# Performance work log

Hardware: AMD Instinct MI355X
Metric: run time of the kernel (lower is better)

Reference implementation:

```python
import jax, jax.numpy as jnp
import numpy as np

NEG_SLOPE = 0.01  # torch F.leaky_relu default


def setup_inputs() -> dict:
    key = jax.random.key(0)
    k1, k2, k3, k4 = jax.random.split(key, 4)
    N, E, R, D = 100000, 1250000, 16, 64
    ego_embed = jax.random.normal(k1, (N, D), dtype=jnp.float32) * 0.1
    relation_weights = jax.random.normal(k2, (R, D, D), dtype=jnp.float32) * (1.0 / np.sqrt(D))
    edge_index = jax.random.randint(k3, (2, E), 0, N, dtype=jnp.int32)
    edge_type = jax.random.randint(k4, (E,), 0, R, dtype=jnp.int32)
    return {"ego_embed": ego_embed, "relation_weights": relation_weights,
            "edge_index": edge_index, "edge_type": edge_type}


def reference(ego_embed, relation_weights, edge_index, edge_type):
    head, tail = edge_index[0], edge_index[1]
    n_entities = ego_embed.shape[0]
    # Transform every node by every relation once ([R,N,D]) instead of
    # materializing the per-edge [E,D,D] weight gather the torch bmm implies;
    # same math: transformed_head[e] = ego_embed[head[e]] @ W[edge_type[e]].
    transformed_all = jnp.einsum('nd,rdk->rnk', ego_embed, relation_weights)
    transformed_head = transformed_all[edge_type, head]        # [E, D]
    tail_emb = ego_embed[tail]                                  # [E, D]
    scores = jax.nn.leaky_relu(jnp.sum(transformed_head * tail_emb, axis=1),
                               negative_slope=NEG_SLOPE)        # [E]
    exp_scores = jnp.exp(scores)                                # unnormalized attention
    denom = jax.ops.segment_sum(exp_scores, head, num_segments=n_entities)[head]
    norm_att = exp_scores / denom                               # segment softmax
    weighted = tail_emb * norm_att[:, None]                     # [E, D]
    # scatter_mean: segment sum / per-segment edge count (clamped to 1)
    summed = jax.ops.segment_sum(weighted, head, num_segments=n_entities)
    counts = jax.ops.segment_sum(jnp.ones_like(exp_scores), head, num_segments=n_entities)
    return summed / jnp.maximum(counts, 1.0)[:, None]
```

## Files before the change

kernel.cpp:

```cpp
#include <hip/hip_runtime.h>
#include <stdint.h>

#define NEG_SLOPE 0.01f
#define HPG 32
#define TSTR 72
#define BSH 8
#define NBMAX 512
#define K1CH 8192
#define CAP2 8192

typedef float f32x4 __attribute__((ext_vector_type(4)));
typedef short short8 __attribute__((ext_vector_type(8)));
typedef unsigned int u32;

#define DPPADD(v, ctrl) ((v) + __int_as_float(__builtin_amdgcn_update_dpp( \
        0, __float_as_int(v), (ctrl), 0xF, 0xF, true)))

__device__ inline short f2bf(float f) {
    union { float f; uint32_t u; } x; x.f = f;
    uint32_t r = x.u + 0x7FFF + ((x.u >> 16) & 1);
    return (short)(r >> 16);
}
__device__ inline float bf2f(unsigned short u) {
    union { uint32_t u; float f; } x; x.u = ((uint32_t)u) << 16; return x.f;
}

__global__ void __launch_bounds__(512) kA(
        const int* __restrict__ head, const int* __restrict__ tail,
        const int* __restrict__ etype, int E, int NB, int nblk,
        u32* __restrict__ staging, int* bucket_cur,
        const float* __restrict__ ego, unsigned short* __restrict__ ego_bf,
        int NE8, const float* __restrict__ rw, short* __restrict__ wfrag,
        int* __restrict__ head_off, int N) {
    int t = threadIdx.x;
    int bid = blockIdx.x;
    if (bid < nblk) {
        __shared__ int lcnt[NBMAX], lbase[NBMAX], lfill[NBMAX];
        for (int b = t; b < NBMAX; b += 512) lcnt[b] = 0;
        __syncthreads();
        long long base = (long long)bid * K1CH;
        short mybk[K1CH / 512];
        u32 myrec[K1CH / 512];
        #pragma unroll
        for (int s = 0; s < K1CH / 512; ++s) {
            long long e = base + t + s * 512;
            int bk = -1; u32 rec = 0;
            if (e < E) {
                int h = head[e];
                bk = h >> BSH;
                rec = (u32)tail[e] | ((u32)etype[e] << 20) | ((u32)(h & 255) << 24);
                atomicAdd(&lcnt[bk], 1);
            }
            mybk[s] = (short)bk; myrec[s] = rec;
        }
        __syncthreads();
        for (int b = t; b < NB; b += 512) {
            int c = lcnt[b];
            lbase[b] = c ? atomicAdd(&bucket_cur[b], c) : 0;
            lfill[b] = 0;
        }
        __syncthreads();
        #pragma unroll
        for (int s = 0; s < K1CH / 512; ++s) {
            int bk = mybk[s];
            if (bk >= 0) {
                int rk = atomicAdd(&lfill[bk], 1);
                int pos = lbase[bk] + rk;
                if (pos >= CAP2) pos = CAP2 - 1;
                staging[(size_t)bk * CAP2 + pos] = myrec[s];
            }
        }
    } else {
        int ib = bid - nblk;
        if (ib == 0 && t == 0) head_off[N] = E;
        if (ib < 16) {
            int r = ib;
            int lane = t & 63;
            int c = lane & 15, q = lane >> 4;
            int pair = t >> 6;
            int t4 = pair >> 1, kh = pair & 1;
            int m = t4 * 16 + c;
            short8 f;
            for (int j = 0; j < 8; ++j) {
                int k = kh * 32 + q * 8 + j;
                f[j] = f2bf(rw[r * 4096 + k * 64 + m]);
            }
            *(short8*)(wfrag + ((size_t)((r * 4 + t4) * 2 + kh) * 64 + lane) * 8) = f;
        }
        int i = ib * 512 + t;
        if (i < NE8) {
            const float4* p = (const float4*)ego + (size_t)i * 2;
            float4 a = p[0], b = p[1];
            short8 v;
            v[0] = f2bf(a.x); v[1] = f2bf(a.y); v[2] = f2bf(a.z); v[3] = f2bf(a.w);
            v[4] = f2bf(b.x); v[5] = f2bf(b.y); v[6] = f2bf(b.z); v[7] = f2bf(b.w);
            *(short8*)(ego_bf + (size_t)i * 8) = v;
        }
    }
}

__global__ void __launch_bounds__(512) kB(
        const u32* __restrict__ staging, const int* __restrict__ bucket_cur,
        int* __restrict__ head_off, int* __restrict__ recs2, int N, int NB) {
    __shared__ int pre[NBMAX];
    __shared__ int lcnt[256], lofs[256], lfill[256];
    __shared__ u32 lrec[CAP2];
    int t = threadIdx.x;
    int b = blockIdx.x;
    if (t < 256) lcnt[t] = 0;
    int v = (t < NB) ? bucket_cur[t] : 0;
    pre[t] = v;
    __syncthreads();
    for (int off = 1; off < 512; off <<= 1) {
        int x = (t >= off) ? pre[t - off] : 0;
        __syncthreads();
        pre[t] += x;
        __syncthreads();
    }
    int cnt_raw = bucket_cur[b];
    int base_g = pre[b] - cnt_raw;
    int cntb = cnt_raw > CAP2 ? CAP2 : cnt_raw;
    int hbase = b << BSH;
    const u32* sb = staging + (size_t)b * CAP2;
    for (int t0 = t; t0 < cntb; t0 += 512) {
        u32 rec = sb[t0];
        lrec[t0] = rec;
        atomicAdd(&lcnt[rec >> 24], 1);
    }
    __syncthreads();
    if (t < 64) {
        int cl[4]; int cs = 0;
        #pragma unroll
        for (int j = 0; j < 4; ++j) { cl[j] = lcnt[t * 4 + j]; cs += cl[j]; }
        int inc = cs;
        for (int off = 1; off < 64; off <<= 1) {
            int u = __shfl_up(inc, off);
            if (t >= off) inc += u;
        }
        int run = inc - cs;
        #pragma unroll
        for (int j = 0; j < 4; ++j) {
            lofs[t * 4 + j] = run; lfill[t * 4 + j] = run; run += cl[j];
        }
    }
    __syncthreads();
    if (t < 256 && hbase + t < N)
        head_off[hbase + t] = base_g + lofs[t];
    for (int t0 = t; t0 < cntb; t0 += 512) {
        u32 rec = lrec[t0];
        int rk = atomicAdd(&lfill[rec >> 24], 1);
        recs2[base_g + rk] = (int)(rec & 0xFFFFFF);
    }
}

__global__ void __launch_bounds__(512, 4) k4_fused(
        const unsigned short* __restrict__ ego_bf,
        const short* __restrict__ wfrag,
        const int* __restrict__ recs2,
        const int* __restrict__ head_off,
        float* __restrict__ out, int N) {
    __shared__ unsigned short T[16 * HPG * TSTR];
    int tid = threadIdx.x;
    int wave = tid >> 6;
    int lane = tid & 63;
    int c = lane & 15, q = lane >> 4;
    int hb = blockIdx.x * HPG;

    for (int t = 0; t < 2; ++t) {
        int r = wave * 2 + t;
        const short* wp = wfrag + (size_t)r * 4096;
        short8 wf[4][2];
        #pragma unroll
        for (int t4 = 0; t4 < 4; ++t4)
            #pragma unroll
            for (int kh = 0; kh < 2; ++kh)
                wf[t4][kh] = *(const short8*)(wp + ((size_t)((t4 * 2 + kh) * 64 + lane)) * 8);
        #pragma unroll
        for (int hf = 0; hf < 2; ++hf) {
            int hrow = hb + hf * 16 + c;
            if (hrow >= N) hrow = N - 1;
            const unsigned short* hr = ego_bf + (size_t)hrow * 64;
            short8 b0 = *(const short8*)(hr + q * 8);
            short8 b1 = *(const short8*)(hr + 32 + q * 8);
            #pragma unroll
            for (int t4 = 0; t4 < 4; ++t4) {
                f32x4 a = {0.f, 0.f, 0.f, 0.f};
                a = __builtin_amdgcn_mfma_f32_16x16x32_bf16(wf[t4][0], b0, a, 0, 0, 0);
                a = __builtin_amdgcn_mfma_f32_16x16x32_bf16(wf[t4][1], b1, a, 0, 0, 0);
                ushort4 us;
                us.x = (unsigned short)f2bf(a[0]);
                us.y = (unsigned short)f2bf(a[1]);
                us.z = (unsigned short)f2bf(a[2]);
                us.w = (unsigned short)f2bf(a[3]);
                *(ushort4*)&T[(size_t)(r * HPG + hf * 16 + c) * TSTR + t4 * 16 + q * 4] = us;
            }
        }
    }
    __syncthreads();

    int hql = wave * 4 + q;
    int h = hb + hql;
    if (h >= N) return;
    int lq = c;
    int g2 = lq >> 3, c8 = lq & 7;
    int qb = q * 16;
    int s0 = head_off[h], s1 = head_off[h + 1];
    int cnt = s1 - s0;
    int nbt = (cnt + 15) >> 4;
    float acc[8] = {0.f, 0.f, 0.f, 0.f, 0.f, 0.f, 0.f, 0.f};
    float den = 0.f;

    auto loadRec = [&](int b) -> int {
        if (b >= nbt) return 0;
        int idx = s0 + b * 16 + lq;
        return (idx < s1) ? recs2[idx] : 0;
    };

    int rjA[8]; short8 rowsA[8];
    int recL1;
    {
        int recL0 = loadRec(0);
        #pragma unroll
        for (int j = 0; j < 8; ++j) rjA[j] = __shfl(recL0, qb + j * 2 + g2);
        #pragma unroll
        for (int j = 0; j < 8; ++j)
            rowsA[j] = *(const short8*)(ego_bf + (size_t)(rjA[j] & 0xFFFFF) * 64 + c8 * 8);
        recL1 = loadRec(1);
    }
    for (int b = 0; b < nbt; ++b) {
        int recL2 = loadRec(b + 2);
        int rjB[8]; short8 rowsB[8];
        #pragma unroll
        for (int j = 0; j < 8; ++j) rjB[j] = __shfl(recL1, qb + j * 2 + g2);
        #pragma unroll
        for (int j = 0; j < 8; ++j)
            rowsB[j] = *(const short8*)(ego_bf + (size_t)(rjB[j] & 0xFFFFF) * 64 + c8 * 8);
        int ng = s1 - (s0 + b * 16); if (ng > 16) ng = 16;
        #pragma unroll
        for (int sIt = 0; sIt < 8; ++sIt) {
            if (sIt * 2 < ng) {
                short8 trw = *(const short8*)&T[(size_t)(((u32)rjA[sIt] >> 20) * HPG + hql) * TSTR + c8 * 8];
                float rf[8];
                float sa = 0.f, sb = 0.f;
                #pragma unroll
                for (int k = 0; k < 4; ++k) {
                    rf[k] = bf2f((unsigned short)rowsA[sIt][k]);
                    sa += rf[k] * bf2f((unsigned short)trw[k]);
                }
                #pragma unroll
                for (int k = 4; k < 8; ++k) {
                    rf[k] = bf2f((unsigned short)rowsA[sIt][k]);
                    sb += rf[k] * bf2f((unsigned short)trw[k]);
                }
                float s = sa + sb;
                s = DPPADD(s, 0xB1);
                s = DPPADD(s, 0x4E);
                s = DPPADD(s, 0x141);
                float lr = s > 0.f ? s : NEG_SLOPE * s;
                float w = (sIt * 2 + g2 < ng) ? __expf(lr) : 0.f;
                den += w;
                #pragma unroll
                for (int k = 0; k < 8; ++k) acc[k] += w * rf[k];
            }
        }
        recL1 = recL2;
        #pragma unroll
        for (int j = 0; j < 8; ++j) { rjA[j] = rjB[j]; rowsA[j] = rowsB[j]; }
    }
    den = DPPADD(den, 0x128);
    #pragma unroll
    for (int k = 0; k < 8; ++k) acc[k] = DPPADD(acc[k], 0x128);
    if (g2 == 0) {
        float sc = (cnt > 0) ? 1.f / (den * (float)cnt) : 0.f;
        float4 v0 = {acc[0] * sc, acc[1] * sc, acc[2] * sc, acc[3] * sc};
        float4 v1 = {acc[4] * sc, acc[5] * sc, acc[6] * sc, acc[7] * sc};
        float* op = out + (size_t)h * 64 + c8 * 8;
        *(float4*)op = v0;
        *(float4*)(op + 4) = v1;
    }
}

extern "C" void kernel_launch(void* const* d_in, const int* in_sizes, int n_in,
                              void* d_out, int out_size, void* d_ws, size_t ws_size,
                              hipStream_t stream) {
    const float* ego = (const float*)d_in[0];
    const float* rw  = (const float*)d_in[1];
    const int* eidx  = (const int*)d_in[2];
    const int* etyp  = (const int*)d_in[3];
    int N = in_sizes[0] / 64;
    int E = in_sizes[3];
    const int* head = eidx;
    const int* tail = eidx + E;
    float* out = (float*)d_out;

    char* ws = (char*)d_ws;
    size_t o = 0;
    auto take = [&](size_t bytes) -> char* {
        char* p = ws + o;
        o = (o + bytes + 255) & ~(size_t)255;
        return p;
    };
    int NB = (N + (1 << BSH) - 1) >> BSH;
    if (NB > NBMAX) NB = NBMAX;
    int nblk = (E + K1CH - 1) / K1CH;
    int NE8 = N * 8;
    int nbI = (NE8 + 511) / 512;
    if (nbI < 16) nbI = 16;
    unsigned short* ego_bf = (unsigned short*)take((size_t)N * 64 * 2);
    short* wfrag    = (short*)take(16 * 4096 * 2);
    int* recs2      = (int*)take((size_t)E * 4);
    u32* staging    = (u32*)take((size_t)NB * CAP2 * 4);
    int* bucket_cur = (int*)take(NBMAX * 4);
    int* head_off   = (int*)take((size_t)(N + 1) * 4);
    (void)ws_size; (void)n_in; (void)out_size;

    hipMemsetAsync(bucket_cur, 0, NBMAX * 4, stream);
    kA<<<nblk + nbI, 512, 0, stream>>>(head, tail, etyp, E, NB, nblk,
                                       staging, bucket_cur,
                                       ego, ego_bf, NE8, rw, wfrag,
                                       head_off, N);
    kB<<<NB, 512, 0, stream>>>(staging, bucket_cur, head_off, recs2, N, NB);
    k4_fused<<<(N + HPG - 1) / HPG, 512, 0, stream>>>(ego_bf, wfrag, recs2,
                                                      head_off, out, N);
}
```

Measured before the change: 180.0 us.

## Halve heads per block and split each head's edges across two lane groups

Each block now covers 16 heads instead of 32, which halves the shared-memory transform table and raises the occupancy hint from 4 to 8 blocks. Each head's edge list is split between two 16-lane groups, and their partial softmax denominators and accumulators are combined with a cross-lane shuffle. This shortens the per-head serial loop and evens out load across degree-skewed heads. In exchange, the per-block 16x64x64 weight MFMA work and the weight-fragment loads are amortized over half as many heads, and the cross-group reduction adds a little overhead.

```diff
diff --git a/kernel.cpp b/kernel.cpp
--- a/kernel.cpp
+++ b/kernel.cpp
@@ -2,7 +2,7 @@
 #include <stdint.h>
 
 #define NEG_SLOPE 0.01f
-#define HPG 32
+#define HPG 16
 #define TSTR 72
 #define BSH 8
 #define NBMAX 512
@@ -153,7 +153,7 @@
     }
 }
 
-__global__ void __launch_bounds__(512, 4) k4_fused(
+__global__ void __launch_bounds__(512, 8) k4_fused(
         const unsigned short* __restrict__ ego_bf,
         const short* __restrict__ wfrag,
         const int* __restrict__ recs2,
@@ -175,45 +175,46 @@
             #pragma unroll
             for (int kh = 0; kh < 2; ++kh)
                 wf[t4][kh] = *(const short8*)(wp + ((size_t)((t4 * 2 + kh) * 64 + lane)) * 8);
-        #pragma unroll
-        for (int hf = 0; hf < 2; ++hf) {
-            int hrow = hb + hf * 16 + c;
-            if (hrow >= N) hrow = N - 1;
-            const unsigned short* hr = ego_bf + (size_t)hrow * 64;
-            short8 b0 = *(const short8*)(hr + q * 8);
-            short8 b1 = *(const short8*)(hr + 32 + q * 8);
-            #pragma unroll
-            for (int t4 = 0; t4 < 4; ++t4) {
-                f32x4 a = {0.f, 0.f, 0.f, 0.f};
-                a = __builtin_amdgcn_mfma_f32_16x16x32_bf16(wf[t4][0], b0, a, 0, 0, 0);
-                a = __builtin_amdgcn_mfma_f32_16x16x32_bf16(wf[t4][1], b1, a, 0, 0, 0);
-                ushort4 us;
-                us.x = (unsigned short)f2bf(a[0]);
-                us.y = (unsigned short)f2bf(a[1]);
-                us.z = (unsigned short)f2bf(a[2]);
-                us.w = (unsigned short)f2bf(a[3]);
-                *(ushort4*)&T[(size_t)(r * HPG + hf * 16 + c) * TSTR + t4 * 16 + q * 4] = us;
-            }
+        int hrow = hb + c;
+        if (hrow >= N) hrow = N - 1;
+        const unsigned short* hr = ego_bf + (size_t)hrow * 64;
+        short8 b0 = *(const short8*)(hr + q * 8);
+        short8 b1 = *(const short8*)(hr + 32 + q * 8);
+        #pragma unroll
+        for (int t4 = 0; t4 < 4; ++t4) {
+            f32x4 a = {0.f, 0.f, 0.f, 0.f};
+            a = __builtin_amdgcn_mfma_f32_16x16x32_bf16(wf[t4][0], b0, a, 0, 0, 0);
+            a = __builtin_amdgcn_mfma_f32_16x16x32_bf16(wf[t4][1], b1, a, 0, 0, 0);
+            ushort4 us;
+            us.x = (unsigned short)f2bf(a[0]);
+            us.y = (unsigned short)f2bf(a[1]);
+            us.z = (unsigned short)f2bf(a[2]);
+            us.w = (unsigned short)f2bf(a[3]);
+            *(ushort4*)&T[(size_t)(r * HPG + c) * TSTR + t4 * 16 + q * 4] = us;
         }
     }
     __syncthreads();
 
-    int hql = wave * 4 + q;
+    int hql = wave * 2 + (q >> 1);
+    int halfsel = q & 1;
     int h = hb + hql;
-    if (h >= N) return;
+    bool act = (h < N);
     int lq = c;
     int g2 = lq >> 3, c8 = lq & 7;
     int qb = q * 16;
-    int s0 = head_off[h], s1 = head_off[h + 1];
-    int cnt = s1 - s0;
+    int s0g = 0, cntF = 0;
+    if (act) { s0g = head_off[h]; cntF = head_off[h + 1] - s0g; }
+    int m = cntF >> 1;
+    int a0 = s0g + (halfsel ? m : 0);
+    int cnt = halfsel ? (cntF - m) : m;
     int nbt = (cnt + 15) >> 4;
     float acc[8] = {0.f, 0.f, 0.f, 0.f, 0.f, 0.f, 0.f, 0.f};
     float den = 0.f;
 
     auto loadRec = [&](int b) -> int {
         if (b >= nbt) return 0;
-        int idx = s0 + b * 16 + lq;
-        return (idx < s1) ? recs2[idx] : 0;
+        int idx = b * 16 + lq;
+        return (idx < cnt) ? recs2[a0 + idx] : 0;
     };
 
     int rjA[8]; short8 rowsA[8];
@@ -235,11 +236,11 @@
         #pragma unroll
         for (int j = 0; j < 8; ++j)
             rowsB[j] = *(const short8*)(ego_bf + (size_t)(rjB[j] & 0xFFFFF) * 64 + c8 * 8);
-        int ng = s1 - (s0 + b * 16); if (ng > 16) ng = 16;
+        int ng = cnt - b * 16; if (ng > 16) ng = 16;
         #pragma unroll
         for (int sIt = 0; sIt < 8; ++sIt) {
             if (sIt * 2 < ng) {
-                short8 trw = *(const short8*)&T[(size_t)(((u32)rjA[sIt] >> 20) * HPG + hql) * TSTR + c8 * 8];
+                short8 trw = *(const short8*)&T[(size_t)((((u32)rjA[sIt] >> 20) & 15) * HPG + hql) * TSTR + c8 * 8];
                 float rf[8];
                 float sa = 0.f, sb = 0.f;
                 #pragma unroll
@@ -270,8 +271,11 @@
     den = DPPADD(den, 0x128);
     #pragma unroll
     for (int k = 0; k < 8; ++k) acc[k] = DPPADD(acc[k], 0x128);
-    if (g2 == 0) {
-        float sc = (cnt > 0) ? 1.f / (den * (float)cnt) : 0.f;
+    den += __shfl_xor(den, 16);
+    #pragma unroll
+    for (int k = 0; k < 8; ++k) acc[k] += __shfl_xor(acc[k], 16);
+    if (act && halfsel == 0 && g2 == 0) {
+        float sc = (cntF > 0) ? 1.f / (den * (float)cntF) : 0.f;
         float4 v0 = {acc[0] * sc, acc[1] * sc, acc[2] * sc, acc[3] * sc};
         float4 v1 = {acc[4] * sc, acc[5] * sc, acc[6] * sc, acc[7] * sc};
         float* op = out + (size_t)h * 64 + c8 * 8;
```

Result: slower. 398.2 us (+121.2%).
